# Kernel tuning notes

Hardware: AMD Instinct MI355X
Metric: run time of the kernel (lower is better)

Reference implementation:

```python
import jax, jax.numpy as jnp
import numpy as np

NEAR, FAR = 0.05, 6.0
STEPSIZE = 0.5
ALPHA_INIT = 1e-6
XYZ_MIN = np.array([-1.0, -1.0, -1.0], np.float32)
XYZ_MAX = np.array([1.0, 1.0, 1.0], np.float32)
WORLD = (160, 160, 160)
VOXEL_SIZE = 2.0 / 160.0  # ((prod span)/num_voxels)^(1/3)
N_SAMPLES = int(np.linalg.norm(np.array(WORLD) + 1) / STEPSIZE) + 1  # 558
ACT_SHIFT = float(np.log(1.0 / (1.0 - ALPHA_INIT) - 1.0))


def setup_inputs() -> dict:
    key = jax.random.key(0)
    k1, k2, k3, k4, k5, k6, k7 = jax.random.split(key, 7)
    rays_o = (jax.random.uniform(k1, (8192, 3), jnp.float32) - 0.5) * 1.2  # inside bbox
    rd = jax.random.normal(k2, (8192, 3), jnp.float32)
    rays_d = rd / jnp.linalg.norm(rd, axis=-1, keepdims=True)
    jitter = jax.random.uniform(k3, (8192, 1), jnp.float32)
    em_modes = jax.random.randint(k4, (8192,), 0, 2, jnp.int32)
    density = jax.random.normal(k5, (1, 160, 160, 160), jnp.float32) * 0.1
    off_color = jax.random.normal(k6, (3, 160, 160, 160), jnp.float32) * 0.1
    emo_color = jax.random.normal(k7, (3, 160, 160, 160), jnp.float32) * 0.1
    return {"rays_o": rays_o, "rays_d": rays_d, "jitter": jitter, "em_modes": em_modes,
            "density": density, "off_color": off_color, "emo_color": emo_color}


def grid_sampler(pts, grid):
    """Trilinear interp, align_corners=True, zero padding. grid [C,Nx,Ny,Nz], pts [...,3] -> [...,C]."""
    C = grid.shape[0]
    sizes = np.array(grid.shape[1:], np.int32)
    lead = pts.shape[:-1]
    t = (pts.reshape(-1, 3) - XYZ_MIN) / (XYZ_MAX - XYZ_MIN)
    idx = t * (jnp.asarray(sizes, pts.dtype) - 1)  # voxel-space coords
    i0 = jnp.floor(idx).astype(jnp.int32)
    f = idx - i0.astype(pts.dtype)
    out = jnp.zeros((i0.shape[0], C), grid.dtype)
    for corner in range(8):
        off = np.array([(corner >> 2) & 1, (corner >> 1) & 1, corner & 1], np.int32)
        ci = i0 + off  # [N,3]
        w = jnp.prod(jnp.where(off[None, :] == 1, f, 1.0 - f), axis=-1)  # [N]
        valid = jnp.all((ci >= 0) & (ci < sizes[None, :]), axis=-1)
        cc = jnp.clip(ci, 0, sizes[None, :] - 1)
        vals = grid[:, cc[:, 0], cc[:, 1], cc[:, 2]].T  # [N,C]
        out = out + (w * valid)[:, None] * vals
    return out.reshape(*lead, C)


def sample_ray(rays_o, rays_d, jitter):
    vec = jnp.where(rays_d == 0, 1e-6, rays_d)
    rate_a = (XYZ_MAX - rays_o) / vec
    rate_b = (XYZ_MIN - rays_o) / vec
    t_min = jnp.clip(jnp.minimum(rate_a, rate_b).max(-1), NEAR, FAR)
    t_max = jnp.clip(jnp.maximum(rate_a, rate_b).min(-1), NEAR, FAR)
    mask_out = t_max <= t_min  # [R]
    rng = jnp.arange(N_SAMPLES, dtype=rays_o.dtype)[None, :] + jitter  # [R,S]
    step = STEPSIZE * VOXEL_SIZE * rng
    interpx = t_min[:, None] + step / jnp.linalg.norm(rays_d, axis=-1, keepdims=True)
    rays_pts = rays_o[:, None, :] + rays_d[:, None, :] * interpx[..., None]  # [R,S,3]
    mask_out = mask_out[:, None] | ((rays_pts < XYZ_MIN) | (rays_pts > XYZ_MAX)).any(-1)
    return rays_pts, mask_out


def reference(rays_o, rays_d, jitter, em_modes, density, off_color, emo_color):
    rays_pts, mask_out = sample_ray(rays_o, rays_d, jitter)
    dens = grid_sampler(rays_pts, density)[..., 0]  # [R,S]
    alpha_all = 1.0 - jnp.exp(-jax.nn.softplus(dens + ACT_SHIFT) * STEPSIZE)
    alpha = jnp.where(mask_out, 0.0, alpha_all)
    p = jnp.clip(1.0 - alpha, 1e-10, None)
    alphainv_cum = jnp.concatenate([jnp.ones_like(p[..., :1]), jnp.cumprod(p, -1)], -1)  # [R,S+1]
    weights = alpha * alphainv_cum[..., :-1]
    on_mask = (em_modes == 1)[:, None, None]
    emo = jax.nn.sigmoid(grid_sampler(rays_pts, emo_color))
    off = jax.nn.sigmoid(grid_sampler(rays_pts, off_color))
    rgb = jnp.where(on_mask, emo, 0.0) + off  # [R,S,3]
    rgb_marched = (weights[..., None] * rgb).sum(-2)  # [R,3]
    return (alphainv_cum, weights, alphainv_cum[..., -1:], rgb, rgb_marched)
```

## Files before the change

kernel.cpp:

```cpp
#include <hip/hip_runtime.h>
#include <math.h>


namespace {
constexpr int   kR   = 8192;
constexpr int   kS   = 558;
constexpr int   kNC  = (kS + 63) / 64;
constexpr int   kG   = 160;
constexpr int   kG3  = kG * kG * kG;
constexpr float kNear = 0.05f;
constexpr float kFar  = 6.0f;
constexpr float kStepWorld = 0.5f * (2.0f / 160.0f);
constexpr float kActShift = -13.815509557963774f;
constexpr float kLog2e = 1.4426950408889634f;
constexpr int   kBX = 80, kBY = 80, kBZ = 40;
constexpr int   kNB = kBX * kBY * kBZ;
constexpr int   kGridWords = kNB * 16;
constexpr int   kXS = kBY * kBZ * 16;
constexpr int   kYS = kBZ * 16;
}

typedef unsigned int nuint4 __attribute__((ext_vector_type(4)));
typedef float        nfloat2 __attribute__((ext_vector_type(2)));
typedef float        nfloat4 __attribute__((ext_vector_type(4)));

__device__ __forceinline__ float fexp(float x) {
  return __builtin_amdgcn_exp2f(x * kLog2e);
}
__device__ __forceinline__ float sigmoidf_(float x) {
  return __builtin_amdgcn_rcpf(1.0f + fexp(-x));
}

__global__ __launch_bounds__(256) void repack_grids(
    const float* __restrict__ density,
    const float* __restrict__ off_c,
    const float* __restrict__ emo_c,
    unsigned* __restrict__ gridA,
    unsigned* __restrict__ gridB)
{
  const int t   = blockIdx.x * blockDim.x + threadIdx.x;
  const int bid = t >> 2;
  const int q   = t & 3;
  if (bid >= kNB) return;
  const int bz = bid % kBZ;
  const int u  = bid / kBZ;
  const int by = u % kBY;
  const int bx = u / kBY;
  const int x  = bx * 2 + (q >> 1);
  const int y  = by * 2 + (q & 1);
  const int z0 = bz * 4;
  const int vbase = (x * kG + y) * kG + z0;

  const nfloat4 d  = __builtin_nontemporal_load((const nfloat4*)(density + vbase));
  const nfloat4 f0 = __builtin_nontemporal_load((const nfloat4*)(off_c + vbase));
  const nfloat4 f1 = __builtin_nontemporal_load((const nfloat4*)(off_c + vbase + kG3));
  const nfloat4 f2 = __builtin_nontemporal_load((const nfloat4*)(off_c + vbase + 2 * kG3));
  const nfloat4 e0 = __builtin_nontemporal_load((const nfloat4*)(emo_c + vbase));
  const nfloat4 e1 = __builtin_nontemporal_load((const nfloat4*)(emo_c + vbase + kG3));
  const nfloat4 e2 = __builtin_nontemporal_load((const nfloat4*)(emo_c + vbase + 2 * kG3));

  nuint4 va, vb;
  #pragma unroll
  for (int lz = 0; lz < 4; ++lz) {
    int qa = __builtin_amdgcn_cvt_pk_fp8_f32(d[lz],  f0[lz], 0,  false);
    qa     = __builtin_amdgcn_cvt_pk_fp8_f32(f1[lz], f2[lz], qa, true);
    int qb = __builtin_amdgcn_cvt_pk_fp8_f32(e0[lz], e1[lz], 0,  false);
    qb     = __builtin_amdgcn_cvt_pk_fp8_f32(e2[lz], 0.0f,   qb, true);
    va[lz] = (unsigned)qa;
    vb[lz] = (unsigned)qb;
  }
  const size_t woff = (size_t)bid * 16 + q * 4;
  __builtin_nontemporal_store(va, (nuint4*)(gridA + woff));
  __builtin_nontemporal_store(vb, (nuint4*)(gridB + woff));
}

__global__ __launch_bounds__(256) void dvgo_fwd(
    const float* __restrict__ rays_o,
    const float* __restrict__ rays_d,
    const float* __restrict__ jitter,
    const int*   __restrict__ em_modes,
    const unsigned* __restrict__ gridA,
    const unsigned* __restrict__ gridB,
    float* __restrict__ out)
{
  const int ray  = blockIdx.x;
  const int wv   = (threadIdx.x >> 6) & 3;
  const int lane = threadIdx.x & 63;

  __shared__ float s_prod[kNC];
  __shared__ float s_acc[4][3];

  const float ox = rays_o[ray * 3 + 0];
  const float oy = rays_o[ray * 3 + 1];
  const float oz = rays_o[ray * 3 + 2];
  const float dx = rays_d[ray * 3 + 0];
  const float dy = rays_d[ray * 3 + 1];
  const float dz = rays_d[ray * 3 + 2];
  const float jit = jitter[ray];
  const bool  on  = (em_modes[ray] == 1);

  const float vx = (dx == 0.0f) ? 1e-6f : dx;
  const float vy = (dy == 0.0f) ? 1e-6f : dy;
  const float vz = (dz == 0.0f) ? 1e-6f : dz;
  const float ivx = __builtin_amdgcn_rcpf(vx);
  const float ivy = __builtin_amdgcn_rcpf(vy);
  const float ivz = __builtin_amdgcn_rcpf(vz);
  const float rax = ( 1.0f - ox) * ivx, rbx = (-1.0f - ox) * ivx;
  const float ray_a = ( 1.0f - oy) * ivy, rby = (-1.0f - oy) * ivy;
  const float raz = ( 1.0f - oz) * ivz, rbz = (-1.0f - oz) * ivz;
  float tmin = fmaxf(fmaxf(fminf(rax, rbx), fminf(ray_a, rby)), fminf(raz, rbz));
  float tmax = fminf(fminf(fmaxf(rax, rbx), fmaxf(ray_a, rby)), fmaxf(raz, rbz));
  tmin = fminf(fmaxf(tmin, kNear), kFar);
  tmax = fminf(fmaxf(tmax, kNear), kFar);
  const bool  ray_out = (tmax <= tmin);
  const float stepc = kStepWorld *
      __builtin_amdgcn_rsqf(dx * dx + dy * dy + dz * dz);

  float* out_ainv = out;
  float* out_w    = out + kR * (kS + 1);
  float* out_last = out_w + kR * kS;
  float* out_rgb  = out_last + kR;
  float* out_rm   = out_rgb + kR * kS * 3;

  const int base_ainv = ray * (kS + 1);
  const int base_w    = ray * kS;

  if (threadIdx.x == 0)
    __builtin_nontemporal_store(1.0f, out_ainv + base_ainv);

  const float c_base = on ? 1.0f : 0.5f;

  auto geom_addr = [&](int s, int wi[8]) -> unsigned long long {
    const bool  ac = (s < kS);
    const float t  = tmin + stepc * ((float)s + jit);
    const float px = fmaf(dx, t, ox);
    const float py = fmaf(dy, t, oy);
    const float pz = fmaf(dz, t, oz);
    const float fx = (px + 1.0f) * 0.5f * (float)(kG - 1);
    const float fy = (py + 1.0f) * 0.5f * (float)(kG - 1);
    const float fz = (pz + 1.0f) * 0.5f * (float)(kG - 1);
    const int ix = (int)floorf(fx);
    const int iy = (int)floorf(fy);
    const int iz = (int)floorf(fz);
    const bool reach = ac &&
        (ix >= -1) && (ix <= kG - 1) &&
        (iy >= -1) && (iy <= kG - 1) &&
        (iz >= -1) && (iz <= kG - 1);
    const int gx0 = min(max(ix, 0), kG - 1),     gx1 = min(max(ix + 1, 0), kG - 1);
    const int gy0 = min(max(iy, 0), kG - 1),     gy1 = min(max(iy + 1, 0), kG - 1);
    const int gz0 = min(max(iz, 0), kG - 1),     gz1 = min(max(iz + 1, 0), kG - 1);
    const int X0 = (gx0 >> 1) * kXS + (gx0 & 1) * 8;
    const int X1 = (gx1 >> 1) * kXS + (gx1 & 1) * 8;
    const int Y0 = (gy0 >> 1) * kYS + (gy0 & 1) * 4;
    const int Y1 = (gy1 >> 1) * kYS + (gy1 & 1) * 4;
    const int Z0 = (gz0 >> 2) * 16 + (gz0 & 3);
    const int Z1 = (gz1 >> 2) * 16 + (gz1 & 3);
    wi[0] = X0 + Y0 + Z0; wi[1] = X0 + Y0 + Z1;
    wi[2] = X0 + Y1 + Z0; wi[3] = X0 + Y1 + Z1;
    wi[4] = X1 + Y0 + Z0; wi[5] = X1 + Y0 + Z1;
    wi[6] = X1 + Y1 + Z0; wi[7] = X1 + Y1 + Z1;
    return __ballot(reach);
  };

  auto geom_w = [&](int s, float w8[8], bool& masked) {
    const float t  = tmin + stepc * ((float)s + jit);
    const float px = fmaf(dx, t, ox);
    const float py = fmaf(dy, t, oy);
    const float pz = fmaf(dz, t, oz);
    const bool inb = (px >= -1.0f) & (px <= 1.0f) &
                     (py >= -1.0f) & (py <= 1.0f) &
                     (pz >= -1.0f) & (pz <= 1.0f);
    masked = ray_out || !inb;
    const float fx = (px + 1.0f) * 0.5f * (float)(kG - 1);
    const float fy = (py + 1.0f) * 0.5f * (float)(kG - 1);
    const float fz = (pz + 1.0f) * 0.5f * (float)(kG - 1);
    const int ix = (int)floorf(fx);
    const int iy = (int)floorf(fy);
    const int iz = (int)floorf(fz);
    const float wx = fx - (float)ix;
    const float wy = fy - (float)iy;
    const float wz = fz - (float)iz;
    const float x0 = 1.0f - wx, y0 = 1.0f - wy, z0 = 1.0f - wz;
    const float wxy00 = x0 * y0, wxy01 = x0 * wy;
    const float wxy10 = wx * y0, wxy11 = wx * wy;
    const bool vx0 = ((unsigned)ix       < (unsigned)kG);
    const bool vx1 = ((unsigned)(ix + 1) < (unsigned)kG);
    const bool vy0 = ((unsigned)iy       < (unsigned)kG);
    const bool vy1 = ((unsigned)(iy + 1) < (unsigned)kG);
    const bool vz0 = ((unsigned)iz       < (unsigned)kG);
    const bool vz1 = ((unsigned)(iz + 1) < (unsigned)kG);
    w8[0] = (vx0 & vy0 & vz0) ? wxy00 * z0 : 0.0f;
    w8[1] = (vx0 & vy0 & vz1) ? wxy00 * wz : 0.0f;
    w8[2] = (vx0 & vy1 & vz0) ? wxy01 * z0 : 0.0f;
    w8[3] = (vx0 & vy1 & vz1) ? wxy01 * wz : 0.0f;
    w8[4] = (vx1 & vy0 & vz0) ? wxy10 * z0 : 0.0f;
    w8[5] = (vx1 & vy0 & vz1) ? wxy10 * wz : 0.0f;
    w8[6] = (vx1 & vy1 & vz0) ? wxy11 * z0 : 0.0f;
    w8[7] = (vx1 & vy1 & vz1) ? wxy11 * wz : 0.0f;
  };

  float incl_a[3], excl_a[3], rr_a[3], gg_a[3], bb_a[3];

  unsigned cua[8], cub[8];
  bool cur_live;
  {
    int wi[8];
    const unsigned long long bal = geom_addr(wv * 64 + lane, wi);
    cur_live = (bal != 0ull);
    if (cur_live) {
      #pragma unroll
      for (int c = 0; c < 8; ++c) cua[c] = gridA[wi[c]];
      if (on) {
        #pragma unroll
        for (int c = 0; c < 8; ++c) cub[c] = gridB[wi[c]];
      }
    }
  }

  #pragma unroll
  for (int k = 0; k < 3; ++k) {
    const int c = wv + 4 * k;
    if (c < kNC) {
      const int s = c * 64 + lane;

      unsigned nua[8], nub[8];
      bool nxt_live = false;
      if (c + 4 < kNC) {
        int wi[8];
        const unsigned long long bal = geom_addr((c + 4) * 64 + lane, wi);
        nxt_live = (bal != 0ull);
        if (nxt_live) {
          #pragma unroll
          for (int q = 0; q < 8; ++q) nua[q] = gridA[wi[q]];
          if (on) {
            #pragma unroll
            for (int q = 0; q < 8; ++q) nub[q] = gridB[wi[q]];
          }
        }
      }

      float incl = 1.0f, excl = 1.0f;
      float rr = c_base, gg = c_base, bb = c_base;

      if (cur_live) {
        float w8[8];
        bool masked;
        geom_w(s, w8, masked);
        float dsum = 0.0f;
        float o0 = 0.0f, o1 = 0.0f, o2 = 0.0f;
        float e0 = 0.0f, e1 = 0.0f, e2 = 0.0f;
        #pragma unroll
        for (int q = 0; q < 8; ++q) {
          const float w = w8[q];
          dsum = fmaf(w, __builtin_amdgcn_cvt_f32_fp8((int)cua[q], 0), dsum);
          o0   = fmaf(w, __builtin_amdgcn_cvt_f32_fp8((int)cua[q], 1), o0);
          o1   = fmaf(w, __builtin_amdgcn_cvt_f32_fp8((int)cua[q], 2), o1);
          o2   = fmaf(w, __builtin_amdgcn_cvt_f32_fp8((int)cua[q], 3), o2);
        }
        if (on) {
          #pragma unroll
          for (int q = 0; q < 8; ++q) {
            const float w = w8[q];
            e0 = fmaf(w, __builtin_amdgcn_cvt_f32_fp8((int)cub[q], 0), e0);
            e1 = fmaf(w, __builtin_amdgcn_cvt_f32_fp8((int)cub[q], 1), e1);
            e2 = fmaf(w, __builtin_amdgcn_cvt_f32_fp8((int)cub[q], 2), e2);
          }
        }

        float p = 1.0f;
        if ((s < kS) && !masked) {
          const float expx = fexp(dsum + kActShift);
          p = fmaxf(__builtin_amdgcn_rsqf(1.0f + expx), 1e-10f);
        }

        incl = p;
        #pragma unroll
        for (int o = 1; o < 64; o <<= 1) {
          const float n = __shfl_up(incl, o, 64);
          if (lane >= o) incl *= n;
        }
        excl = __shfl_up(incl, 1, 64);
        if (lane == 0) excl = 1.0f;

        rr = sigmoidf_(o0);
        gg = sigmoidf_(o1);
        bb = sigmoidf_(o2);
        if (on) {
          rr += sigmoidf_(e0);
          gg += sigmoidf_(e1);
          bb += sigmoidf_(e2);
        }
      }

      if (s < kS) {
        const int rb = (base_w + s) * 3;
        nfloat2 rg;
        rg.x = rr; rg.y = gg;
        __builtin_nontemporal_store(rg, (nfloat2*)(out_rgb + rb));
        __builtin_nontemporal_store(bb, out_rgb + rb + 2);
      }

      incl_a[k] = incl; excl_a[k] = excl;
      rr_a[k] = rr; gg_a[k] = gg; bb_a[k] = bb;

      const float prod = __shfl(incl, 63, 64);
      if (lane == 0) s_prod[c] = prod;

      cur_live = nxt_live;
      #pragma unroll
      for (int q = 0; q < 8; ++q) cua[q] = nua[q];
      if (on) {
        #pragma unroll
        for (int q = 0; q < 8; ++q) cub[q] = nub[q];
      }
    }
  }

  __syncthreads();

  float sp[kNC];
  #pragma unroll
  for (int i = 0; i < kNC; ++i) sp[i] = s_prod[i];

  float accr = 0.0f, accg = 0.0f, accb = 0.0f;
  #pragma unroll
  for (int k = 0; k < 3; ++k) {
    const int c = wv + 4 * k;
    if (c < kNC) {
      float carry = 1.0f;
      #pragma unroll
      for (int i = 0; i < kNC; ++i) carry *= (i < c) ? sp[i] : 1.0f;
      const int s = c * 64 + lane;
      const float anext = carry * incl_a[k];
      const float aprev = carry * excl_a[k];
      const float wgt   = aprev - anext;
      if (s < kS) {
        __builtin_nontemporal_store(anext, out_ainv + base_ainv + s + 1);
        __builtin_nontemporal_store(wgt, out_w + base_w + s);
        accr = fmaf(wgt, rr_a[k], accr);
        accg = fmaf(wgt, gg_a[k], accg);
        accb = fmaf(wgt, bb_a[k], accb);
      }
    }
  }

  #pragma unroll
  for (int o = 32; o > 0; o >>= 1) {
    accr += __shfl_xor(accr, o, 64);
    accg += __shfl_xor(accg, o, 64);
    accb += __shfl_xor(accb, o, 64);
  }
  if (lane == 0) {
    s_acc[wv][0] = accr;
    s_acc[wv][1] = accg;
    s_acc[wv][2] = accb;
  }
  __syncthreads();

  if (threadIdx.x == 0) {
    out_rm[ray * 3 + 0] = s_acc[0][0] + s_acc[1][0] + s_acc[2][0] + s_acc[3][0];
    out_rm[ray * 3 + 1] = s_acc[0][1] + s_acc[1][1] + s_acc[2][1] + s_acc[3][1];
    out_rm[ray * 3 + 2] = s_acc[0][2] + s_acc[1][2] + s_acc[2][2] + s_acc[3][2];
    float tot = 1.0f;
    #pragma unroll
    for (int i = 0; i < kNC; ++i) tot *= sp[i];
    out_last[ray] = tot;
  }
}

extern "C" void kernel_launch(void* const* d_in, const int* in_sizes, int n_in,
                              void* d_out, int out_size, void* d_ws, size_t ws_size,
                              hipStream_t stream) {
  const float* rays_o  = (const float*)d_in[0];
  const float* rays_d  = (const float*)d_in[1];
  const float* jitter  = (const float*)d_in[2];
  const int*   em      = (const int*)d_in[3];
  const float* density = (const float*)d_in[4];
  const float* off_c   = (const float*)d_in[5];
  const float* emo_c   = (const float*)d_in[6];
  float* out = (float*)d_out;

  unsigned* gridA = (unsigned*)d_ws;
  unsigned* gridB = gridA + kGridWords;
  (void)ws_size;

  hipLaunchKernelGGL(repack_grids, dim3((kNB * 4 + 255) / 256), dim3(256), 0,
                     stream, density, off_c, emo_c, gridA, gridB);

  hipLaunchKernelGGL(dvgo_fwd, dim3(kR), dim3(256), 0, stream,
                     rays_o, rays_d, jitter, em, gridA, gridB, out);
}
```

Baseline: 218.0 us.

## Bucket rays by direction and origin octant to improve grid cache locality

Adds a single-block kernel that sorts rays into 64 buckets keyed by direction-sign and origin-octant, producing a permutation. The main kernel maps block IDs through this permutation, with an XCD-aware interleave (bid&7) so each chiplet processes a contiguous slice of similar rays. The goal is for concurrently running blocks to touch overlapping grid regions and get better L2 hit rates. It adds one extra serial launch using a single workgroup and an indirect load per block.

```diff
diff --git a/kernel.cpp b/kernel.cpp
--- a/kernel.cpp
+++ b/kernel.cpp
@@ -29,6 +29,48 @@
 }
 __device__ __forceinline__ float sigmoidf_(float x) {
   return __builtin_amdgcn_rcpf(1.0f + fexp(-x));
+}
+
+__global__ __launch_bounds__(1024) void bucket_rays(
+    const float* __restrict__ rays_o,
+    const float* __restrict__ rays_d,
+    int* __restrict__ perm)
+{
+  __shared__ unsigned cnt[64];
+  __shared__ unsigned off[64];
+  const int tid = threadIdx.x;
+  if (tid < 64) cnt[tid] = 0u;
+  __syncthreads();
+
+  int keys[8];
+  #pragma unroll
+  for (int i = 0; i < 8; ++i) {
+    const int r = tid * 8 + i;
+    const float dx = rays_d[r * 3 + 0];
+    const float dy = rays_d[r * 3 + 1];
+    const float dz = rays_d[r * 3 + 2];
+    const float ox = rays_o[r * 3 + 0];
+    const float oy = rays_o[r * 3 + 1];
+    const float oz = rays_o[r * 3 + 2];
+    const int kd = ((dx < 0.0f) ? 4 : 0) | ((dy < 0.0f) ? 2 : 0) | ((dz < 0.0f) ? 1 : 0);
+    const int ko = ((ox < 0.0f) ? 4 : 0) | ((oy < 0.0f) ? 2 : 0) | ((oz < 0.0f) ? 1 : 0);
+    keys[i] = kd * 8 + ko;
+    atomicAdd(&cnt[keys[i]], 1u);
+  }
+  __syncthreads();
+
+  if (tid == 0) {
+    unsigned run = 0;
+    for (int k = 0; k < 64; ++k) { off[k] = run; run += cnt[k]; }
+  }
+  __syncthreads();
+
+  #pragma unroll
+  for (int i = 0; i < 8; ++i) {
+    const int r = tid * 8 + i;
+    const unsigned pos = atomicAdd(&off[keys[i]], 1u);
+    perm[pos] = r;
+  }
 }
 
 __global__ __launch_bounds__(256) void repack_grids(
@@ -81,9 +123,11 @@
     const int*   __restrict__ em_modes,
     const unsigned* __restrict__ gridA,
     const unsigned* __restrict__ gridB,
+    const int*   __restrict__ perm,
     float* __restrict__ out)
 {
-  const int ray  = blockIdx.x;
+  const int bid  = blockIdx.x;
+  const int ray  = perm[((bid & 7) << 10) | (bid >> 3)];
   const int wv   = (threadIdx.x >> 6) & 3;
   const int lane = threadIdx.x & 63;
 
@@ -382,11 +426,14 @@
 
   unsigned* gridA = (unsigned*)d_ws;
   unsigned* gridB = gridA + kGridWords;
+  int*      perm  = (int*)(gridB + kGridWords);
   (void)ws_size;
 
+  hipLaunchKernelGGL(bucket_rays, dim3(1), dim3(1024), 0, stream,
+                     rays_o, rays_d, perm);
   hipLaunchKernelGGL(repack_grids, dim3((kNB * 4 + 255) / 256), dim3(256), 0,
                      stream, density, off_c, emo_c, gridA, gridB);
 
   hipLaunchKernelGGL(dvgo_fwd, dim3(kR), dim3(256), 0, stream,
-                     rays_o, rays_d, jitter, em, gridA, gridB, out);
-}
+                     rays_o, rays_d, jitter, em, gridA, gridB, perm, out);
+}
```

After: 232.5 us. 1.07x slower.
